# Optimization experiments

Measured on AMD Instinct MI355X. Metric: run time of the kernel, lower is better.

The kernel has to match this reference:

```python
import jax, jax.numpy as jnp
import numpy as np

N, IN_DIM, E_RAW, N_GRAPHS, HEADS = 50000, 128, 800000, 256, 2
NEG_ATT, NEG_ACT, EPS = 0.2, 0.01, 1e-5


def _gat(x, src, dst, W, a_src, a_dst, bias):
    # PyG GATConv: x' = xW per head; alpha = softmax_over_dst(leaky_relu(a_s.h_src + a_d.h_dst, 0.2))
    H, C = a_src.shape
    n = x.shape[0]
    h = (x @ W).reshape(n, H, C)                                  # [N,H,C]
    al_s = jnp.einsum('nhc,hc->nh', h, a_src)                     # [N,H]
    al_d = jnp.einsum('nhc,hc->nh', h, a_dst)                     # [N,H]
    e = jax.nn.leaky_relu(al_s[src] + al_d[dst], NEG_ATT)         # [E,H]
    m = jax.ops.segment_max(e, dst, num_segments=n)               # per-dst max (stable softmax)
    ee = jnp.exp(e - m[dst])
    s = jax.ops.segment_sum(ee, dst, num_segments=n)
    alpha = ee / (s[dst] + 1e-16)                                 # [E,H]
    out = jax.ops.segment_sum(h[src] * alpha[:, :, None], dst, num_segments=n)
    return out.reshape(n, H * C) + bias


def _bn(x, g, b):
    # training-mode BatchNorm1d over nodes (biased variance), eps=1e-5
    m = jnp.mean(x, 0)
    v = jnp.var(x, 0)
    return (x - m) * jax.lax.rsqrt(v + EPS) * g + b


def setup_inputs() -> dict:
    key = jax.random.key(0)
    ks = jax.random.split(key, 20)
    H, C1, C2, C3 = HEADS, 32, 64, 128
    rn = lambda i, sh, s=0.05: jax.random.normal(ks[i], sh, jnp.float32) * s
    inp = dict(
        x=jax.random.normal(ks[0], (N, IN_DIM), jnp.float32),
        edge_index=jax.random.randint(ks[1], (2, E_RAW), 0, N, jnp.int32),
        edge_weigth=jax.random.uniform(ks[2], (E_RAW,), jnp.float32),
        batch=jnp.sort(jax.random.randint(ks[3], (N,), 0, N_GRAPHS, jnp.int32)),
        W1=rn(4, (IN_DIM, H * C1)), a_src1=rn(5, (H, C1)), a_dst1=rn(6, (H, C1)),
        b1=jnp.zeros((H * C1,), jnp.float32), g1=jnp.ones((H * C1,), jnp.float32), be1=jnp.zeros((H * C1,), jnp.float32),
        W2=rn(7, (H * C1, H * C2)), a_src2=rn(8, (H, C2)), a_dst2=rn(9, (H, C2)),
        b2=jnp.zeros((H * C2,), jnp.float32), g2=jnp.ones((H * C2,), jnp.float32), be2=jnp.zeros((H * C2,), jnp.float32),
        W3=rn(10, (H * C2, H * C3)), a_src3=rn(11, (H, C3)), a_dst3=rn(12, (H, C3)),
        b3=jnp.zeros((H * C3,), jnp.float32), g3=jnp.ones((H * C3,), jnp.float32), be3=jnp.zeros((H * C3,), jnp.float32),
        Wc1=rn(13, (H * C1 + H * C2 + H * C3, 128)), bc1=jnp.zeros((128,), jnp.float32),
        Wc2=rn(14, (128, 64)), bc2=jnp.zeros((64,), jnp.float32),
        Wc3=rn(15, (64, 2)), bc3=jnp.zeros((2,), jnp.float32),
    )
    return inp


def reference(x, edge_index, edge_weigth, batch,
              W1, a_src1, a_dst1, b1, g1, be1,
              W2, a_src2, a_dst2, b2, g2, be2,
              W3, a_src3, a_dst3, b3, g3, be3,
              Wc1, bc1, Wc2, bc2, Wc3, bc3):
    n = x.shape[0]
    loops = jnp.arange(n, dtype=edge_index.dtype)  # GATConv add_self_loops=True
    src = jnp.concatenate([edge_index[0], loops])
    dst = jnp.concatenate([edge_index[1], loops])
    lr = lambda t: jax.nn.leaky_relu(t, NEG_ACT)
    x1 = lr(_bn(_gat(x, src, dst, W1, a_src1, a_dst1, b1), g1, be1))
    x2 = lr(_bn(_gat(x1, src, dst, W2, a_src2, a_dst2, b2), g2, be2))
    x3 = lr(_bn(_gat(x2, src, dst, W3, a_src3, a_dst3, b3), g3, be3))
    p = jnp.concatenate([
        jax.ops.segment_sum(x1, batch, num_segments=N_GRAPHS),
        jax.ops.segment_sum(x2, batch, num_segments=N_GRAPHS),
        jax.ops.segment_sum(x3, batch, num_segments=N_GRAPHS)], axis=1)
    h = lr(p @ Wc1 + bc1)
    h = lr(h @ Wc2 + bc2)
    return h @ Wc3 + bc3
```

## Files before the change

### kernel.cpp

```cpp
#include <hip/hip_runtime.h>
#include <hip/hip_fp16.h>
#include <math.h>

#define N_NODES 50000
#define E_RAW_N 800000
#define E_TOT   (E_RAW_N + N_NODES)
#define NGRAPH  256
#define POOL_F  448
#define SCAN_B  196
#define NSLICE  4
#define MBLK    391
#define EBLK    3321
#define PBLK    391

using f16x8 = __attribute__((ext_vector_type(8))) _Float16;
using f32x4 = __attribute__((ext_vector_type(4))) float;


template<int K, int F>
__device__ void do_wt(const float* __restrict__ W, __half* __restrict__ WT, int blk) {
    int i = blk * 256 + threadIdx.x;
    if (i >= F * (K / 8)) return;
    int f = i / (K / 8);
    int kb = (i % (K / 8)) * 8;
    __half tmp[8];
#pragma unroll
    for (int j = 0; j < 8; ++j) tmp[j] = __float2half(W[(size_t)(kb + j) * F + f]);
    *reinterpret_cast<uint4*>(WT + (size_t)f * K + kb) = *reinterpret_cast<uint4*>(tmp);
}


__global__ void k_init(int* __restrict__ deg, float* __restrict__ p,
                       float* __restrict__ bn,
                       const float* __restrict__ W1, const float* __restrict__ W2,
                       const float* __restrict__ W3, __half* __restrict__ WT1,
                       __half* __restrict__ WT2, __half* __restrict__ WT3) {
    int b = blockIdx.x;
    if (b < 448) {
        int i = b * 256 + threadIdx.x;
        if (i < N_NODES) deg[i] = 0;
        if (i < NGRAPH * POOL_F) p[i] = 0.f;
        if (i < NSLICE * 512 * 3) bn[i] = 0.f;
    } else {
        int wb = b - 448;
        if (wb < 4)       do_wt<128, 64>(W1, WT1, wb);
        else if (wb < 8)  do_wt<64, 128>(W2, WT2, wb - 4);
        else              do_wt<128, 256>(W3, WT3, wb - 8);
    }
}


__device__ inline void degrank_body(int bid, const int* __restrict__ dst_raw,
                                    int* __restrict__ deg, int* __restrict__ rank) {
    int e = bid * 256 + threadIdx.x;
    if (e >= E_TOT) return;
    int d = (e < E_RAW_N) ? dst_raw[e] : (e - E_RAW_N);
    rank[e] = atomicAdd(&deg[d], 1);
}

__global__ void k_scan1(const int* __restrict__ deg, int* __restrict__ bsum) {
    __shared__ int red[256];
    int i = blockIdx.x * 256 + threadIdx.x;
    int v = (i < N_NODES) ? deg[i] : 0;
    red[threadIdx.x] = v;
    __syncthreads();
    for (int o = 128; o > 0; o >>= 1) {
        if (threadIdx.x < o) red[threadIdx.x] += red[threadIdx.x + o];
        __syncthreads();
    }
    if (threadIdx.x == 0) bsum[blockIdx.x] = red[0];
}

__global__ void k_scan3(const int* __restrict__ deg, const int* __restrict__ bsum,
                        int* __restrict__ rowstart) {
    __shared__ int pre[256];
    __shared__ int s[256];
    int tid = threadIdx.x;
    pre[tid] = (tid < (int)blockIdx.x) ? bsum[tid] : 0;
    int i = blockIdx.x * 256 + tid;
    int v = (i < N_NODES) ? deg[i] : 0;
    s[tid] = v;
    __syncthreads();
    for (int o = 128; o > 0; o >>= 1) {
        if (tid < o) pre[tid] += pre[tid + o];
        __syncthreads();
    }
    for (int o = 1; o < 256; o <<= 1) {
        int t = (tid >= o) ? s[tid - o] : 0;
        __syncthreads();
        s[tid] += t;
        __syncthreads();
    }
    if (i < N_NODES) rowstart[i] = pre[0] + s[tid] - v;
    if (i == 0) rowstart[N_NODES] = E_TOT;
}

__global__ void k_fill(const int* __restrict__ ei, const int* __restrict__ rowstart,
                       const int* __restrict__ rank, int* __restrict__ adj) {
    int e = blockIdx.x * blockDim.x + threadIdx.x;
    if (e >= E_TOT) return;
    int s, d;
    if (e < E_RAW_N) { s = ei[e]; d = ei[E_RAW_N + e]; }
    else             { s = d = e - E_RAW_N; }
    adj[rowstart[d] + rank[e]] = s;
}


template<int F>
__device__ void bnpool_body(int bid, const __half* __restrict__ x,
                            const float* __restrict__ bnP, const float* __restrict__ g,
                            const float* __restrict__ be, const int* __restrict__ batch,
                            float* __restrict__ p, int poff) {
    constexpr int F2 = F / 2;
    constexpr int NGRP = 512 / F;
    constexpr int NPB = 128;
    int f2 = threadIdx.x % F2;
    int grp = threadIdx.x / F2;
    int f = 2 * f2;
    const float invN = 1.f / (float)N_NODES;
    float sm0 = 0.f, sm1 = 0.f, sq0 = 0.f, sq1 = 0.f;
#pragma unroll
    for (int s = 0; s < NSLICE; ++s) {
        sm0 += bnP[s * 2 * F + f];     sm1 += bnP[s * 2 * F + f + 1];
        sq0 += bnP[s * 2 * F + F + f]; sq1 += bnP[s * 2 * F + F + f + 1];
    }
    float m0 = sm0 * invN, m1 = sm1 * invN;
    float v0 = sq0 * invN - m0 * m0;
    float v1 = sq1 * invN - m1 * m1;
    float sc0 = rsqrtf(v0 + 1e-5f) * g[f];
    float sc1 = rsqrtf(v1 + 1e-5f) * g[f + 1];
    float bb0 = be[f] - m0 * sc0;
    float bb1 = be[f + 1] - m1 * sc1;
    int n0 = bid * NPB;
    int nend = n0 + NPB; if (nend > N_NODES) nend = N_NODES;
    int n = n0 + grp;
    if (n >= nend) return;
    float p0 = 0.f, p1 = 0.f;
    int cg = batch[n];
    for (; n < nend; n += NGRP) {
        float2 xv = __half22float2(*reinterpret_cast<const __half2*>(x + (size_t)n * F + f));
        float y0 = xv.x * sc0 + bb0; y0 = y0 > 0.f ? y0 : 0.01f * y0;
        float y1 = xv.y * sc1 + bb1; y1 = y1 > 0.f ? y1 : 0.01f * y1;
        int bg = batch[n];
        if (bg != cg) {
            atomicAdd(&p[cg * POOL_F + poff + f], p0);
            atomicAdd(&p[cg * POOL_F + poff + f + 1], p1);
            p0 = p1 = 0.f; cg = bg;
        }
        p0 += y0; p1 += y1;
    }
    atomicAdd(&p[cg * POOL_F + poff + f], p0);
    atomicAdd(&p[cg * POOL_F + poff + f + 1], p1);
}

template<int F>
__global__ void k_bnpool(const __half* __restrict__ x, const float* __restrict__ bnP,
                         const float* __restrict__ g, const float* __restrict__ be,
                         const int* __restrict__ batch, float* __restrict__ p, int poff) {
    bnpool_body<F>(blockIdx.x, x, bnP, g, be, batch, p, poff);
}


template<int K, int F, bool BNIN, bool SPLIT, typename TIN, typename TOUT, int SIDE>
__global__ void __launch_bounds__(256) k_mfma(
        const TIN* __restrict__ x, const __half* __restrict__ WT,
        const float* __restrict__ bnP,
        const float* __restrict__ g, const float* __restrict__ be,
        const float* __restrict__ a_src, const float* __restrict__ a_dst,
        void* __restrict__ hout, float* __restrict__ al_s, float* __restrict__ al_d,
        const int* __restrict__ dst_raw, int* __restrict__ deg, int* __restrict__ rank,
        const int* __restrict__ batch, float* __restrict__ pp, int poff) {
    if constexpr (SIDE == 1) {
        if (blockIdx.x >= MBLK) { degrank_body(blockIdx.x - MBLK, dst_raw, deg, rank); return; }
    } else if constexpr (SIDE == 2) {
        if (blockIdx.x >= MBLK) {
            if (blockIdx.y == 0)
                bnpool_body<K>(blockIdx.x - MBLK, (const __half*)x, bnP, g, be, batch, pp, poff);
            return;
        }
    }
    constexpr int FH = SPLIT ? F / 2 : F;
    constexpr int NF = FH / 16;
    constexpr int KS = K / 32;
    constexpr int MT = 2;
    constexpr int C  = F / 2;
    const int hd  = SPLIT ? (int)blockIdx.y : 0;
    const int fof = hd * C;
    __shared__ float scs[K], bbs[K];
    int tid = threadIdx.x;
    if constexpr (BNIN) {
        const float invN = 1.f / (float)N_NODES;
        for (int i = tid; i < K; i += 256) {
            float sm = 0.f, sq = 0.f;
#pragma unroll
            for (int s = 0; s < NSLICE; ++s) {
                sm += bnP[s * 2 * K + i];
                sq += bnP[s * 2 * K + K + i];
            }
            float mean = sm * invN;
            float var  = sq * invN - mean * mean;
            float sc = rsqrtf(var + 1e-5f) * g[i];
            scs[i] = sc;
            bbs[i] = be[i] - mean * sc;
        }
        __syncthreads();
    }
    int wave = tid >> 6, lane = tid & 63;
    int col = lane & 15;
    int kg  = lane >> 4;
    long n_base = ((long)blockIdx.x * 4 + wave) * (MT * 16);
    if (n_base >= N_NODES) return;

    f32x4 acc[MT][NF];
#pragma unroll
    for (int m = 0; m < MT; ++m)
#pragma unroll
        for (int t = 0; t < NF; ++t) acc[m][t] = (f32x4){0.f, 0.f, 0.f, 0.f};

    for (int ks = 0; ks < KS; ++ks) {
        int kb = ks * 32 + kg * 8;
        f16x8 af[MT];
#pragma unroll
        for (int m = 0; m < MT; ++m) {
            long nrow = n_base + m * 16 + col;
            if (nrow >= N_NODES) nrow = N_NODES - 1;
            if constexpr (sizeof(TIN) == 2) {
                uint4 u = *reinterpret_cast<const uint4*>((const __half*)x + nrow * K + kb);
                if constexpr (BNIN) {
                    const __half* hp = reinterpret_cast<const __half*>(&u);
                    f16x8 a;
#pragma unroll
                    for (int j = 0; j < 8; ++j) {
                        float y = __half2float(hp[j]) * scs[kb + j] + bbs[kb + j];
                        y = y > 0.f ? y : 0.01f * y;
                        a[j] = (_Float16)y;
                    }
                    af[m] = a;
                } else {
                    af[m] = *reinterpret_cast<const f16x8*>(&u);
                }
            } else {
                const float* xp = (const float*)x + nrow * K + kb;
                float4 v0 = *reinterpret_cast<const float4*>(xp);
                float4 v1 = *reinterpret_cast<const float4*>(xp + 4);
                f16x8 a;
                a[0] = (_Float16)v0.x; a[1] = (_Float16)v0.y;
                a[2] = (_Float16)v0.z; a[3] = (_Float16)v0.w;
                a[4] = (_Float16)v1.x; a[5] = (_Float16)v1.y;
                a[6] = (_Float16)v1.z; a[7] = (_Float16)v1.w;
                af[m] = a;
            }
        }
#pragma unroll
        for (int t = 0; t < NF; ++t) {
            f16x8 bf = *reinterpret_cast<const f16x8*>(WT + (size_t)(fof + t * 16 + col) * K + kb);
            acc[0][t] = __builtin_amdgcn_mfma_f32_16x16x32_f16(bf, af[0], acc[0][t], 0, 0, 0);
            if constexpr (MT > 1)
                acc[1][t] = __builtin_amdgcn_mfma_f32_16x16x32_f16(bf, af[1], acc[1][t], 0, 0, 0);
        }
    }

#pragma unroll
    for (int m = 0; m < MT; ++m) {
        int node_i = (int)(n_base + m * 16 + col);
        bool ok = node_i < N_NODES;
#pragma unroll
        for (int t = 0; t < NF; ++t) {
            int fb = fof + t * 16 + kg * 4;
            if (ok) {
                if constexpr (sizeof(TOUT) == 1) {
                    int pk0 = __builtin_amdgcn_cvt_pk_fp8_f32(acc[m][t][0], acc[m][t][1], 0, false);
                    int pk1 = __builtin_amdgcn_cvt_pk_fp8_f32(acc[m][t][2], acc[m][t][3], 0, false);
                    unsigned u = ((unsigned)pk0 & 0xffffu) | ((unsigned)pk1 << 16);
                    *reinterpret_cast<unsigned*>((unsigned char*)hout + (size_t)node_i * F + fb) = u;
                } else {
                    __half2 p0 = __floats2half2_rn(acc[m][t][0], acc[m][t][1]);
                    __half2 p1 = __floats2half2_rn(acc[m][t][2], acc[m][t][3]);
                    uint2 u;
                    u.x = *reinterpret_cast<unsigned int*>(&p0);
                    u.y = *reinterpret_cast<unsigned int*>(&p1);
                    *reinterpret_cast<uint2*>((__half*)hout + (size_t)node_i * F + fb) = u;
                }
            }
        }
        if constexpr (SPLIT) {
            float ss = 0.f, sd = 0.f;
#pragma unroll
            for (int t = 0; t < NF; ++t) {
#pragma unroll
                for (int r = 0; r < 4; ++r) {
                    int f = fof + t * 16 + kg * 4 + r;
                    ss += acc[m][t][r] * a_src[f];
                    sd += acc[m][t][r] * a_dst[f];
                }
            }
            ss += __shfl_xor(ss, 16); ss += __shfl_xor(ss, 32);
            sd += __shfl_xor(sd, 16); sd += __shfl_xor(sd, 32);
            if (kg == 0 && ok) {
                al_s[node_i * 2 + hd] = ss;
                al_d[node_i * 2 + hd] = sd;
            }
        } else {
            float ss0 = 0.f, sd0 = 0.f, ss1 = 0.f, sd1 = 0.f;
#pragma unroll
            for (int t = 0; t < NF; ++t) {
#pragma unroll
                for (int r = 0; r < 4; ++r) {
                    int f = t * 16 + kg * 4 + r;
                    float v = acc[m][t][r];
                    if (t < NF / 2) { ss0 += v * a_src[f]; sd0 += v * a_dst[f]; }
                    else            { ss1 += v * a_src[f]; sd1 += v * a_dst[f]; }
                }
            }
            ss0 += __shfl_xor(ss0, 16); ss0 += __shfl_xor(ss0, 32);
            sd0 += __shfl_xor(sd0, 16); sd0 += __shfl_xor(sd0, 32);
            ss1 += __shfl_xor(ss1, 16); ss1 += __shfl_xor(ss1, 32);
            sd1 += __shfl_xor(sd1, 16); sd1 += __shfl_xor(sd1, 32);
            if (kg == 0 && ok) {
                al_s[node_i * 2]     = ss0; al_s[node_i * 2 + 1] = ss1;
                al_d[node_i * 2]     = sd0; al_d[node_i * 2 + 1] = sd1;
            }
        }
    }
}


template<bool FP8> struct PayT;
template<> struct PayT<false> { using T = uint4; };
template<> struct PayT<true>  { using T = uint2; };

template<bool FP8>
__device__ inline void accum8(typename PayT<FP8>::T u, float ee, float acc[8]) {
    if constexpr (FP8) {
        auto f0 = __builtin_amdgcn_cvt_pk_f32_fp8(u.x, false);
        auto f1 = __builtin_amdgcn_cvt_pk_f32_fp8(u.x, true);
        auto f2 = __builtin_amdgcn_cvt_pk_f32_fp8(u.y, false);
        auto f3 = __builtin_amdgcn_cvt_pk_f32_fp8(u.y, true);
        acc[0] += ee * f0[0]; acc[1] += ee * f0[1];
        acc[2] += ee * f1[0]; acc[3] += ee * f1[1];
        acc[4] += ee * f2[0]; acc[5] += ee * f2[1];
        acc[6] += ee * f3[0]; acc[7] += ee * f3[1];
    } else {
        float2 f0 = __half22float2(*reinterpret_cast<const __half2*>(&u.x));
        float2 f1 = __half22float2(*reinterpret_cast<const __half2*>(&u.y));
        float2 f2 = __half22float2(*reinterpret_cast<const __half2*>(&u.z));
        float2 f3 = __half22float2(*reinterpret_cast<const __half2*>(&u.w));
        acc[0] += ee * f0.x; acc[1] += ee * f0.y;
        acc[2] += ee * f1.x; acc[3] += ee * f1.y;
        acc[4] += ee * f2.x; acc[5] += ee * f2.y;
        acc[6] += ee * f3.x; acc[7] += ee * f3.y;
    }
}

template<int F, int C, bool FP8>
__global__ void __launch_bounds__(256) k_gather(
        const int* __restrict__ rowstart, const int* __restrict__ adj,
        const void* __restrict__ hv, const float* __restrict__ al_s,
        const float* __restrict__ al_d, const float* __restrict__ bias,
        __half* __restrict__ xpre) {
    using LT = typename PayT<FP8>::T;
    constexpr int HPL = 8;
    constexpr int LPE = F / HPL;
    constexpr int EPI = 64 / LPE;
    constexpr int UNR = (EPI >= 8) ? 4 : (16 / EPI);
    constexpr int STEP = UNR * EPI;
    constexpr unsigned RSH = FP8 ? 8 : ((F == 64) ? 7 : 8);
    int wave = (blockIdx.x * 256 + threadIdx.x) >> 6;
    int lane = threadIdx.x & 63;
    if (wave >= N_NODES) return;
    int n = wave;
    int rs = rowstart[n], re = rowstart[n + 1];
    float2 aldv = *reinterpret_cast<const float2*>(al_d + n * 2);

    const int es = lane / LPE;
    const int fl = lane % LPE;
    const unsigned fi = fl * HPL;
    const int hd = (fi >= C) ? 1 : 0;
    const float alh = hd ? aldv.y : aldv.x;
    const char* base = (const char*)hv;
    const char* alsb = (const char*)al_s;
    const unsigned fioff = FP8 ? fi : fi * 2;

    float acc[HPL];
#pragma unroll
    for (int j = 0; j < HPL; ++j) acc[j] = 0.f;
    float seh = 0.f;

    int nsteps = (re - rs + STEP - 1) / STEP;
    unsigned sN[UNR];
#pragma unroll
    for (int u = 0; u < UNR; ++u) {
        int e = rs + u * EPI + es;
        sN[u] = (unsigned)adj[min(e, re - 1)];
    }
    for (int t = 0; t < nsteps; ++t) {
        int ibase = rs + t * STEP;
        unsigned sC[UNR];
#pragma unroll
        for (int u = 0; u < UNR; ++u) sC[u] = sN[u];
        if (t + 1 < nsteps) {
            int nb = ibase + STEP;
#pragma unroll
            for (int u = 0; u < UNR; ++u) {
                int e = nb + u * EPI + es;
                sN[u] = (unsigned)adj[min(e, re - 1)];
            }
        }
        float alsN[UNR];
        LT hvN[UNR];
#pragma unroll
        for (int u = 0; u < UNR; ++u) {
            alsN[u] = *reinterpret_cast<const float*>(alsb + ((sC[u] << 3) | (unsigned)(hd << 2)));
            hvN[u] = *reinterpret_cast<const LT*>(base + ((sC[u] << RSH) + fioff));
        }
#pragma unroll
        for (int u = 0; u < UNR; ++u) {
            bool valid = (ibase + u * EPI + es) < re;
            float v = alsN[u] + alh; v = v > 0.f ? v : 0.2f * v;
            v = fminf(v, 80.f);
            float ee = valid ? __expf(v) : 0.f;
            seh += ee;
            accum8<FP8>(hvN[u], ee, acc);
        }
    }

#pragma unroll
    for (int o = LPE; o < 64; o <<= 1) {
        seh += __shfl_xor(seh, o);
#pragma unroll
        for (int j = 0; j < HPL; ++j) acc[j] += __shfl_xor(acc[j], o);
    }

    if (es == 0) {
        float inv = 1.f / (seh + 1e-16f);
        const float* bp = bias + fi;
        __half2 o0 = __floats2half2_rn(acc[0] * inv + bp[0], acc[1] * inv + bp[1]);
        __half2 o1 = __floats2half2_rn(acc[2] * inv + bp[2], acc[3] * inv + bp[3]);
        __half2 o2 = __floats2half2_rn(acc[4] * inv + bp[4], acc[5] * inv + bp[5]);
        __half2 o3 = __floats2half2_rn(acc[6] * inv + bp[6], acc[7] * inv + bp[7]);
        uint4 u;
        u.x = *reinterpret_cast<unsigned int*>(&o0);
        u.y = *reinterpret_cast<unsigned int*>(&o1);
        u.z = *reinterpret_cast<unsigned int*>(&o2);
        u.w = *reinterpret_cast<unsigned int*>(&o3);
        *reinterpret_cast<uint4*>(xpre + (size_t)n * F + fi) = u;
    }
}


template<int F>
__global__ void __launch_bounds__(256) k_bnstats(const __half* __restrict__ x,
        float* __restrict__ bnP) {
    constexpr int SLOTS = F / 8;
    constexpr int RPI   = 256 / SLOTS;
    __shared__ float ls[256][8];
    int tid = threadIdx.x;
    int slot = tid % SLOTS;
    int r0 = tid / SLOTS;
    int slice = blockIdx.x & (NSLICE - 1);
    float s[8], q[8];
#pragma unroll
    for (int j = 0; j < 8; ++j) { s[j] = 0.f; q[j] = 0.f; }
    int stride = gridDim.x * RPI;
    for (int n = blockIdx.x * RPI + r0; n < N_NODES; n += stride) {
        uint4 u = *reinterpret_cast<const uint4*>(x + (size_t)n * F + slot * 8);
        float2 f0 = __half22float2(*reinterpret_cast<__half2*>(&u.x));
        float2 f1 = __half22float2(*reinterpret_cast<__half2*>(&u.y));
        float2 f2 = __half22float2(*reinterpret_cast<__half2*>(&u.z));
        float2 f3 = __half22float2(*reinterpret_cast<__half2*>(&u.w));
        float v[8] = {f0.x, f0.y, f1.x, f1.y, f2.x, f2.y, f3.x, f3.y};
#pragma unroll
        for (int j = 0; j < 8; ++j) { s[j] += v[j]; q[j] += v[j] * v[j]; }
    }
#pragma unroll
    for (int j = 0; j < 8; ++j) ls[tid][j] = s[j];
    __syncthreads();
    if (tid < F) {
        int sl = tid / 8, j = tid % 8;
        float t = 0.f;
        for (int r = 0; r < RPI; ++r) t += ls[r * SLOTS + sl][j];
        atomicAdd(&bnP[slice * 2 * F + tid], t);
    }
    __syncthreads();
#pragma unroll
    for (int j = 0; j < 8; ++j) ls[tid][j] = q[j];
    __syncthreads();
    if (tid < F) {
        int sl = tid / 8, j = tid % 8;
        float t = 0.f;
        for (int r = 0; r < RPI; ++r) t += ls[r * SLOTS + sl][j];
        atomicAdd(&bnP[slice * 2 * F + F + tid], t);
    }
}


__global__ void k_mlp(const float* __restrict__ p, const float* __restrict__ Wc1,
                      const float* __restrict__ bc1, const float* __restrict__ Wc2,
                      const float* __restrict__ bc2, const float* __restrict__ Wc3,
                      const float* __restrict__ bc3, float* __restrict__ out) {
    __shared__ float pr[POOL_F];
    __shared__ float h1[128];
    __shared__ float h2[64];
    int g = blockIdx.x, tid = threadIdx.x;
    for (int i = tid; i < POOL_F; i += 128) pr[i] = p[g * POOL_F + i];
    __syncthreads();
    float a = bc1[tid];
    for (int k = 0; k < POOL_F; ++k) a += pr[k] * Wc1[k * 128 + tid];
    a = a > 0.f ? a : 0.01f * a;
    h1[tid] = a;
    __syncthreads();
    if (tid < 64) {
        float b = bc2[tid];
        for (int k = 0; k < 128; ++k) b += h1[k] * Wc2[k * 64 + tid];
        b = b > 0.f ? b : 0.01f * b;
        h2[tid] = b;
    }
    __syncthreads();
    if (tid < 2) {
        float c = bc3[tid];
        for (int k = 0; k < 64; ++k) c += h2[k] * Wc3[k * 2 + tid];
        out[g * 2 + tid] = c;
    }
}


extern "C" void kernel_launch(void* const* d_in, const int* in_sizes, int n_in,
                              void* d_out, int out_size, void* d_ws, size_t ws_size,
                              hipStream_t stream) {
    const float* x    = (const float*)d_in[0];
    const int*   ei   = (const int*)d_in[1];
    const int*   batch= (const int*)d_in[3];
    const float* W1  = (const float*)d_in[4];
    const float* as1 = (const float*)d_in[5];
    const float* ad1 = (const float*)d_in[6];
    const float* b1  = (const float*)d_in[7];
    const float* g1  = (const float*)d_in[8];
    const float* be1 = (const float*)d_in[9];
    const float* W2  = (const float*)d_in[10];
    const float* as2 = (const float*)d_in[11];
    const float* ad2 = (const float*)d_in[12];
    const float* b2  = (const float*)d_in[13];
    const float* g2  = (const float*)d_in[14];
    const float* be2 = (const float*)d_in[15];
    const float* W3  = (const float*)d_in[16];
    const float* as3 = (const float*)d_in[17];
    const float* ad3 = (const float*)d_in[18];
    const float* b3  = (const float*)d_in[19];
    const float* g3  = (const float*)d_in[20];
    const float* be3 = (const float*)d_in[21];
    const float* Wc1 = (const float*)d_in[22];
    const float* bc1 = (const float*)d_in[23];
    const float* Wc2 = (const float*)d_in[24];
    const float* bc2 = (const float*)d_in[25];
    const float* Wc3 = (const float*)d_in[26];
    const float* bc3 = (const float*)d_in[27];
    float* out = (float*)d_out;

    char* wsb = (char*)d_ws;
    size_t off = 0;
    auto alloc = [&](size_t b) -> void* {
        void* pp = wsb + off;
        off += (b + 255) & ~(size_t)255;
        return pp;
    };
    int*    adj      = (int*)alloc((size_t)E_TOT * 4);
    int*    rank     = (int*)alloc((size_t)E_TOT * 4);
    int*    rowstart = (int*)alloc((size_t)(N_NODES + 1) * 4);
    int*    deg      = (int*)alloc((size_t)N_NODES * 4);
    int*    bsum     = (int*)alloc(256 * 4);
    float*  al_s     = (float*)alloc((size_t)N_NODES * 2 * 4);
    float*  al_d     = (float*)alloc((size_t)N_NODES * 2 * 4);
    float*  bn1      = (float*)alloc(NSLICE * 512 * 4);
    float*  bn2      = (float*)alloc(NSLICE * 512 * 4);
    float*  bn3      = (float*)alloc(NSLICE * 512 * 4);
    float*  p        = (float*)alloc((size_t)NGRAPH * POOL_F * 4);
    __half* WT1      = (__half*)alloc((size_t)64 * 128 * 2);
    __half* WT2      = (__half*)alloc((size_t)128 * 64 * 2);
    __half* WT3      = (__half*)alloc((size_t)256 * 128 * 2);
    __half* hbuf     = (__half*)alloc((size_t)N_NODES * 128 * 2);
    unsigned char* h8buf = (unsigned char*)alloc((size_t)N_NODES * 256);
    __half* xbuf     = (__half*)alloc((size_t)N_NODES * 256 * 2);

    k_init<<<472, 256, 0, stream>>>(deg, p, bn1, W1, W2, W3, WT1, WT2, WT3);

    int wb = (N_NODES + 3) / 4;
    const int sb = 480;

    k_mfma<128, 64, false, false, float, __half, 1><<<MBLK + EBLK, 256, 0, stream>>>(
        x, WT1, nullptr, nullptr, nullptr, as1, ad1, hbuf, al_s, al_d,
        ei + E_RAW_N, deg, rank, nullptr, nullptr, 0);
    k_scan1<<<SCAN_B, 256, 0, stream>>>(deg, bsum);
    k_scan3<<<SCAN_B, 256, 0, stream>>>(deg, bsum, rowstart);
    k_fill<<<EBLK, 256, 0, stream>>>(ei, rowstart, rank, adj);

    k_gather<64, 32, false><<<wb, 256, 0, stream>>>(rowstart, adj, hbuf, al_s, al_d, b1, xbuf);
    k_bnstats<64><<<sb, 256, 0, stream>>>(xbuf, bn1);

    k_mfma<64, 128, true, true, __half, __half, 2><<<dim3(MBLK + PBLK, 2), 256, 0, stream>>>(
        xbuf, WT2, bn1, g1, be1, as2, ad2, hbuf, al_s, al_d,
        nullptr, nullptr, nullptr, batch, p, 0);
    k_gather<128, 64, false><<<wb, 256, 0, stream>>>(rowstart, adj, hbuf, al_s, al_d, b2, xbuf);
    k_bnstats<128><<<sb, 256, 0, stream>>>(xbuf, bn2);

    k_mfma<128, 256, true, true, __half, unsigned char, 2><<<dim3(MBLK + PBLK, 2), 256, 0, stream>>>(
        xbuf, WT3, bn2, g2, be2, as3, ad3, h8buf, al_s, al_d,
        nullptr, nullptr, nullptr, batch, p, 64);
    k_gather<256, 128, true><<<wb, 256, 0, stream>>>(rowstart, adj, h8buf, al_s, al_d, b3, xbuf);
    k_bnstats<256><<<sb, 256, 0, stream>>>(xbuf, bn3);

    k_bnpool<256><<<PBLK, 256, 0, stream>>>(xbuf, bn3, g3, be3, batch, p, 192);
    k_mlp<<<NGRAPH, 128, 0, stream>>>(p, Wc1, bc1, Wc2, bc2, Wc3, bc3, out);
}
```

Measured before the change: 276.8 us.

## Share edge index and attention weights across lanes via shuffles; use fp16 layer-3 payload

The gather kernel now has each lane load one neighbour index and compute its attention exponent once per head. The values are then broadcast to the feature lanes with warp shuffles, instead of every lane group reloading adj and al_s and recomputing exp. Layer 3 also switches its node-feature payload from fp8 to fp16, which doubles the gathered bytes per edge but removes the fp8 quantisation and its conversion cost. The row-shift constant is generalised so the payload width follows F and the precision flag.

```diff
diff --git a/kernel.cpp b/kernel.cpp
--- a/kernel.cpp
+++ b/kernel.cpp
@@ -364,7 +364,7 @@
     constexpr int EPI = 64 / LPE;
     constexpr int UNR = (EPI >= 8) ? 4 : (16 / EPI);
     constexpr int STEP = UNR * EPI;
-    constexpr unsigned RSH = FP8 ? 8 : ((F == 64) ? 7 : 8);
+    constexpr unsigned RSH = (F == 64 ? 6u : (F == 128 ? 7u : 8u)) + (FP8 ? 0u : 1u);
     int wave = (blockIdx.x * 256 + threadIdx.x) >> 6;
     int lane = threadIdx.x & 63;
     if (wave >= N_NODES) return;
@@ -376,51 +376,58 @@
     const int fl = lane % LPE;
     const unsigned fi = fl * HPL;
     const int hd = (fi >= C) ? 1 : 0;
-    const float alh = hd ? aldv.y : aldv.x;
     const char* base = (const char*)hv;
     const char* alsb = (const char*)al_s;
     const unsigned fioff = FP8 ? fi : fi * 2;
 
+    const int ek  = lane & 31;
+    const int ehd = lane >> 5;
+    const float aldOwn = ehd ? aldv.y : aldv.x;
+
     float acc[HPL];
 #pragma unroll
     for (int j = 0; j < HPL; ++j) acc[j] = 0.f;
     float seh = 0.f;
 
     int nsteps = (re - rs + STEP - 1) / STEP;
-    unsigned sN[UNR];
-#pragma unroll
-    for (int u = 0; u < UNR; ++u) {
-        int e = rs + u * EPI + es;
-        sN[u] = (unsigned)adj[min(e, re - 1)];
-    }
+
+    auto mkEE = [&](unsigned s, int ib) -> float {
+        float als = 0.f;
+        if (ek < STEP)
+            als = *reinterpret_cast<const float*>(alsb + ((s << 3) | (unsigned)(ehd << 2)));
+        float v = als + aldOwn;
+        v = v > 0.f ? v : 0.2f * v;
+        v = fminf(v, 80.f);
+        return ((ib + ek) < re && ek < STEP) ? __expf(v) : 0.f;
+    };
+
+    unsigned sOwn = (unsigned)adj[min(rs + ek, re - 1)];
+    float eeOwn = mkEE(sOwn, rs);
+
     for (int t = 0; t < nsteps; ++t) {
         int ibase = rs + t * STEP;
-        unsigned sC[UNR];
-#pragma unroll
-        for (int u = 0; u < UNR; ++u) sC[u] = sN[u];
+        unsigned sCur = sOwn;
+        float eeCur = eeOwn;
         if (t + 1 < nsteps) {
-            int nb = ibase + STEP;
-#pragma unroll
-            for (int u = 0; u < UNR; ++u) {
-                int e = nb + u * EPI + es;
-                sN[u] = (unsigned)adj[min(e, re - 1)];
-            }
-        }
-        float alsN[UNR];
-        LT hvN[UNR];
+            sOwn = (unsigned)adj[min(ibase + STEP + ek, re - 1)];
+            eeOwn = mkEE(sOwn, ibase + STEP);
+        }
+        unsigned sU[UNR];
+#pragma unroll
+        for (int u = 0; u < UNR; ++u)
+            sU[u] = (unsigned)__shfl((int)sCur, u * EPI + es);
+        LT hvU[UNR];
+#pragma unroll
+        for (int u = 0; u < UNR; ++u)
+            hvU[u] = *reinterpret_cast<const LT*>(base + ((size_t)(sU[u] << RSH) + fioff));
+        float eeU[UNR];
+#pragma unroll
+        for (int u = 0; u < UNR; ++u)
+            eeU[u] = __shfl(eeCur, (hd << 5) | (u * EPI + es));
 #pragma unroll
         for (int u = 0; u < UNR; ++u) {
-            alsN[u] = *reinterpret_cast<const float*>(alsb + ((sC[u] << 3) | (unsigned)(hd << 2)));
-            hvN[u] = *reinterpret_cast<const LT*>(base + ((sC[u] << RSH) + fioff));
-        }
-#pragma unroll
-        for (int u = 0; u < UNR; ++u) {
-            bool valid = (ibase + u * EPI + es) < re;
-            float v = alsN[u] + alh; v = v > 0.f ? v : 0.2f * v;
-            v = fminf(v, 80.f);
-            float ee = valid ? __expf(v) : 0.f;
-            seh += ee;
-            accum8<FP8>(hvN[u], ee, acc);
+            seh += eeU[u];
+            accum8<FP8>(hvU[u], eeU[u], acc);
         }
     }
 
@@ -577,8 +584,7 @@
     __half* WT1      = (__half*)alloc((size_t)64 * 128 * 2);
     __half* WT2      = (__half*)alloc((size_t)128 * 64 * 2);
     __half* WT3      = (__half*)alloc((size_t)256 * 128 * 2);
-    __half* hbuf     = (__half*)alloc((size_t)N_NODES * 128 * 2);
-    unsigned char* h8buf = (unsigned char*)alloc((size_t)N_NODES * 256);
+    __half* hbuf     = (__half*)alloc((size_t)N_NODES * 256 * 2);
     __half* xbuf     = (__half*)alloc((size_t)N_NODES * 256 * 2);
 
     k_init<<<472, 256, 0, stream>>>(deg, p, bn1, W1, W2, W3, WT1, WT2, WT3);
@@ -602,10 +608,10 @@
     k_gather<128, 64, false><<<wb, 256, 0, stream>>>(rowstart, adj, hbuf, al_s, al_d, b2, xbuf);
     k_bnstats<128><<<sb, 256, 0, stream>>>(xbuf, bn2);
 
-    k_mfma<128, 256, true, true, __half, unsigned char, 2><<<dim3(MBLK + PBLK, 2), 256, 0, stream>>>(
-        xbuf, WT3, bn2, g2, be2, as3, ad3, h8buf, al_s, al_d,
+    k_mfma<128, 256, true, true, __half, __half, 2><<<dim3(MBLK + PBLK, 2), 256, 0, stream>>>(
+        xbuf, WT3, bn2, g2, be2, as3, ad3, hbuf, al_s, al_d,
         nullptr, nullptr, nullptr, batch, p, 64);
-    k_gather<256, 128, true><<<wb, 256, 0, stream>>>(rowstart, adj, h8buf, al_s, al_d, b3, xbuf);
+    k_gather<256, 128, false><<<wb, 256, 0, stream>>>(rowstart, adj, hbuf, al_s, al_d, b3, xbuf);
     k_bnstats<256><<<sb, 256, 0, stream>>>(xbuf, bn3);
 
     k_bnpool<256><<<PBLK, 256, 0, stream>>>(xbuf, bn3, g3, be3, batch, p, 192);
```

After: 300.8 us. 1.09x slower.
